# Kernel optimization log

Hardware: AMD Instinct MI355X
Metric: run time of the kernel (lower is better)

## Reference

```python
import jax, jax.numpy as jnp
import numpy as np

NUM_HEADS = 16
NHID = 64
D = NUM_HEADS * NHID  # 1024, also keys/query/values dim and out_dim
SL, BS = 2048, 32


def setup_inputs() -> dict:
    key = jax.random.key(0)
    ks = jax.random.split(key, 7)
    s = 1.0 / np.sqrt(D)
    return {
        "query": jax.random.normal(ks[0], (BS, D), jnp.float32),
        "keys": jax.random.normal(ks[1], (SL, BS, D), jnp.float32),
        "values": jax.random.normal(ks[2], (SL, BS, D), jnp.float32),
        "Wq": jax.random.normal(ks[3], (D, D), jnp.float32) * s,
        "Wk": jax.random.normal(ks[4], (D, D), jnp.float32) * s,
        "Wv": jax.random.normal(ks[5], (D, D), jnp.float32) * s,
        "Wo": jax.random.normal(ks[6], (D, D), jnp.float32) * s,
    }


def reference(query, keys, values, Wq, Wk, Wv, Wo):
    sl, bs, _ = keys.shape
    qp = query @ Wq.T                       # [bs, H*nhid]
    kp = keys @ Wk.T                        # [sl, bs, H*nhid]
    vp = values @ Wv.T                      # [sl, bs, H*nhid]
    # elementwise multiplicative score, reduced per head
    dot = (qp * kp).reshape(sl, bs, NUM_HEADS, NHID).sum(-1) / np.sqrt(NHID)
    # NOTE: original uses log_softmax (not softmax) over the sequence dim
    w = jax.nn.log_softmax(dot, axis=0)[..., None]        # [sl, bs, H, 1]
    attn = (w * vp.reshape(sl, bs, NUM_HEADS, NHID)).sum(0)  # [bs, H, nhid]
    return attn.reshape(bs, -1) @ Wo.T                     # [bs, D]
```

## Files before the change

kernel.cpp:

```cpp
#include <hip/hip_runtime.h>

#define SL  2048
#define BSZ 32
#define DIM 1024
#define NH  16
#define HD  64

typedef __attribute__((ext_vector_type(4))) float f32x4;
typedef __attribute__((ext_vector_type(8))) short s16x8;

static __device__ __forceinline__ short f2bf(float f) {
    union { float f; unsigned u; } v; v.f = f;
    unsigned r = (v.u + 0x7fffu + ((v.u >> 16) & 1u)) >> 16;
    return (short)r;
}

template<bool DUAL>
__global__ __launch_bounds__(256) void k_gemm(const float* __restrict__ A,
                                              const float* __restrict__ A2,
                                              const float* __restrict__ W,
                                              float* __restrict__ O,
                                              int rmul, int hsel) {
    int oc = blockIdx.x & 15;
    int b  = blockIdx.x >> 4;
    int wv = __builtin_amdgcn_readfirstlane(threadIdx.x >> 6);
    int lane = threadIdx.x & 63;
    int o = oc * 64 + lane;
    int row = b * rmul + (hsel ? oc : 0);
    const float* arow  = A + (size_t)row * DIM + wv * 256;
    const float* a2row = DUAL ? (A2 + (size_t)row * DIM + wv * 256) : nullptr;
    const float* wrow  = W + (size_t)o * DIM + wv * 256;
    f32x4 acc = {0.f, 0.f, 0.f, 0.f};
#pragma unroll 4
    for (int k = 0; k < 256; k += 4) {
        f32x4 a = *(const f32x4*)(arow + k);
        if (DUAL) a += *(const f32x4*)(a2row + k);
        f32x4 w = *(const f32x4*)(wrow + k);
        acc += a * w;
    }
    __shared__ float red[4][64];
    red[wv][lane] = acc[0] + acc[1] + acc[2] + acc[3];
    __syncthreads();
    int t = threadIdx.x;
    if (t < 64)
        O[(size_t)b * DIM + oc * 64 + t] = red[0][t] + red[1][t] + red[2][t] + red[3][t];
}

__global__ __launch_bounds__(256) void k_ut(const float* __restrict__ qp,
                                            const float* __restrict__ Wk,
                                            short* __restrict__ u) {
    int idx = blockIdx.x;
    int jc = idx & 15;
    int h  = (idx >> 4) & 15;
    int bg = idx >> 8;
    int wv = __builtin_amdgcn_readfirstlane(threadIdx.x >> 6);
    int lane = threadIdx.x & 63;
    int b = bg * 4 + wv;
    int j = jc * 64 + lane;
    const float* qrow = qp + (size_t)b * DIM + h * HD;
    const float* wcol = Wk + (size_t)(h * HD) * DIM + j;
    float acc = 0.f;
#pragma unroll 8
    for (int i = 0; i < HD; ++i) acc += qrow[i] * wcol[(size_t)i * DIM];
    u[((size_t)(b * NH + h)) * DIM + j] = f2bf(acc * 0.125f);
}

__global__ __launch_bounds__(256, 4) void k_dot(const float* __restrict__ keys,
                                                const short* __restrict__ u,
                                                float* __restrict__ dot) {
    int b  = blockIdx.x & 31;
    int s0 = (blockIdx.x >> 5) * 64;
    __shared__ short ulds[NH][DIM + 8];
    {
        const uint4* src = (const uint4*)(u + (size_t)b * NH * DIM);
        for (int idx = threadIdx.x; idx < NH * DIM / 8; idx += 256) {
            int row = idx >> 7;
            int col = (idx & 127) * 8;
            *(uint4*)&ulds[row][col] = src[idx];
        }
    }
    __syncthreads();
    int lane = threadIdx.x & 63;
    int wave = threadIdx.x >> 6;
    int lrow = lane & 15;
    int kgrp = lane >> 4;
    f32x4 acc = {0.f, 0.f, 0.f, 0.f};
    const float* ka = keys + ((size_t)(s0 + wave * 16 + lrow) * BSZ + b) * DIM;
#pragma unroll 4
    for (int k0 = 0; k0 < DIM; k0 += 32) {
        int kj = k0 + kgrp * 8;
        s16x8 bf = *(const s16x8*)&ulds[lrow][kj];
        f32x4 a0 = *(const f32x4*)(ka + kj);
        f32x4 a1 = *(const f32x4*)(ka + kj + 4);
        s16x8 af;
        af[0]=f2bf(a0[0]); af[1]=f2bf(a0[1]); af[2]=f2bf(a0[2]); af[3]=f2bf(a0[3]);
        af[4]=f2bf(a1[0]); af[5]=f2bf(a1[1]); af[6]=f2bf(a1[2]); af[7]=f2bf(a1[3]);
        acc = __builtin_amdgcn_mfma_f32_16x16x32_bf16(af, bf, acc, 0, 0, 0);
    }
    size_t obase = ((size_t)b * SL + (s0 + wave * 16 + kgrp * 4)) * NH + lrow;
#pragma unroll
    for (int r = 0; r < 4; ++r)
        dot[obase + (size_t)r * NH] = acc[r];
}

__global__ __launch_bounds__(1024) void k_red(const float* __restrict__ dot,
                                              float* __restrict__ T) {
    int b = blockIdx.x, t = threadIdx.x;
    const f32x4* base = (const f32x4*)(dot + (size_t)b * SL * NH);
    __shared__ f32x4 red[1024];
    __shared__ float Mh[16];
    f32x4 m = {-1e30f, -1e30f, -1e30f, -1e30f};
#pragma unroll
    for (int k = 0; k < 8; ++k) {
        f32x4 v = base[t + k * 1024];
        m[0]=fmaxf(m[0],v[0]); m[1]=fmaxf(m[1],v[1]);
        m[2]=fmaxf(m[2],v[2]); m[3]=fmaxf(m[3],v[3]);
    }
    red[t] = m;
    __syncthreads();
    for (int s = 512; s >= 4; s >>= 1) {
        if (t < s) {
            f32x4 a = red[t], c = red[t + s];
            a[0]=fmaxf(a[0],c[0]); a[1]=fmaxf(a[1],c[1]);
            a[2]=fmaxf(a[2],c[2]); a[3]=fmaxf(a[3],c[3]);
            red[t] = a;
        }
        __syncthreads();
    }
    if (t < 4) { f32x4 mm = red[t]; for (int i = 0; i < 4; ++i) Mh[t*4+i] = mm[i]; }
    __syncthreads();
    int hq = t & 3;
    f32x4 M4;
    M4[0]=Mh[hq*4]; M4[1]=Mh[hq*4+1]; M4[2]=Mh[hq*4+2]; M4[3]=Mh[hq*4+3];
    f32x4 ssum = {0.f,0.f,0.f,0.f};
#pragma unroll
    for (int k = 0; k < 8; ++k) {
        f32x4 v = base[t + k * 1024];
        ssum[0]+=__expf(v[0]-M4[0]); ssum[1]+=__expf(v[1]-M4[1]);
        ssum[2]+=__expf(v[2]-M4[2]); ssum[3]+=__expf(v[3]-M4[3]);
    }
    __syncthreads();
    red[t] = ssum;
    __syncthreads();
    for (int s = 512; s >= 4; s >>= 1) {
        if (t < s) { f32x4 a = red[t]; a += red[t + s]; red[t] = a; }
        __syncthreads();
    }
    if (t < 4) {
        f32x4 ss = red[t];
        for (int i = 0; i < 4; ++i)
            T[b * NH + t * 4 + i] = Mh[t * 4 + i] + __logf(ss[i]);
    }
}

__global__ __launch_bounds__(256, 4) void k_z(const float* __restrict__ values,
                                              const float* __restrict__ w,
                                              const float* __restrict__ T,
                                              float* __restrict__ z) {
    int x  = blockIdx.x;
    int b  = x & 31;
    int jc = (x >> 5) & 15;
    int sh = x >> 9;
    int t  = threadIdx.x;
    int ssub = t >> 4;
    int jq = t & 15;
    int j = jc * 64 + jq * 4;
    int wv = __builtin_amdgcn_readfirstlane(t >> 6);
    int lane = t & 63;

    __shared__ float wlds[128 * 16];
    __shared__ f32x4 redW[4][16][16];
    __shared__ f32x4 redV[4][16];

    f32x4 acc[NH];
#pragma unroll
    for (int h = 0; h < NH; ++h) acc[h] = (f32x4){0.f,0.f,0.f,0.f};
    f32x4 accV = {0.f,0.f,0.f,0.f};

    const float* vbase = values + (size_t)b * DIM + j;
    const float* wbase = w + ((size_t)b * SL + sh * 1024) * NH;

    for (int ph = 0; ph < 8; ++ph) {
        if (ph) __syncthreads();
        {
            const f32x4* src = (const f32x4*)(wbase + ph * 128 * NH);
            f32x4* dst = (f32x4*)wlds;
            dst[t]       = src[t];
            dst[t + 256] = src[t + 256];
        }
        __syncthreads();
        int sbase = sh * 1024 + ph * 128;
#pragma unroll 4
        for (int it = 0; it < 8; ++it) {
            int s_loc = it * 16 + ssub;
            f32x4 v = *(const f32x4*)(vbase + (size_t)(sbase + s_loc) * (BSZ * DIM));
            const float* wr = wlds + s_loc * 16;
#pragma unroll
            for (int h = 0; h < NH; ++h) {
                float wh = wr[h];
                acc[h] += v * wh;
            }
            accV += v;
        }
    }

#pragma unroll
    for (int h = 0; h < NH; ++h) {
#pragma unroll
        for (int e = 0; e < 4; ++e) {
            float x0 = acc[h][e];
            x0 += __shfl_xor(x0, 16);
            x0 += __shfl_xor(x0, 32);
            acc[h][e] = x0;
        }
    }
#pragma unroll
    for (int e = 0; e < 4; ++e) {
        float x0 = accV[e];
        x0 += __shfl_xor(x0, 16);
        x0 += __shfl_xor(x0, 32);
        accV[e] = x0;
    }
    if (lane < 16) {
#pragma unroll
        for (int h = 0; h < NH; ++h) redW[wv][h][lane] = acc[h];
        redV[wv][lane] = accV;
    }
    __syncthreads();
    int h2 = t >> 4, q = t & 15;
    f32x4 sumW = redW[0][h2][q] + redW[1][h2][q] + redW[2][h2][q] + redW[3][h2][q];
    f32x4 sumV = redV[0][q] + redV[1][q] + redV[2][q] + redV[3][q];
    float Th = T[b * NH + h2];
    f32x4 zv = sumW - Th * sumV;
    float* zp = z + (size_t)sh * (BSZ * NH * DIM);
    *(f32x4*)(zp + ((size_t)(b * NH + h2)) * DIM + jc * 64 + q * 4) = zv;
}

extern "C" void kernel_launch(void* const* d_in, const int* in_sizes, int n_in,
                              void* d_out, int out_size, void* d_ws, size_t ws_size,
                              hipStream_t stream) {
    const float* query  = (const float*)d_in[0];
    const float* keys   = (const float*)d_in[1];
    const float* values = (const float*)d_in[2];
    const float* Wq = (const float*)d_in[3];
    const float* Wk = (const float*)d_in[4];
    const float* Wv = (const float*)d_in[5];
    const float* Wo = (const float*)d_in[6];
    float* out = (float*)d_out;

    char* ws = (char*)d_ws;
    float* qp   = (float*)(ws + 0);
    short* u    = (short*)(ws + (128 << 10));
    float* dotb = (float*)(ws + (128 << 10) + (1 << 20));
    float* z0   = (float*)(ws + (128 << 10) + (5 << 20));
    float* z1   = (float*)(ws + (128 << 10) + (7 << 20));
    float* attn = (float*)(ws + (128 << 10) + (9 << 20));
    float* T    = (float*)(ws + (256 << 10) + (9 << 20));

    hipLaunchKernelGGL(k_gemm<false>, dim3(512),  dim3(256), 0, stream, query, nullptr, Wq, qp, 1, 0);
    hipLaunchKernelGGL(k_ut,          dim3(2048), dim3(256), 0, stream, qp, Wk, u);
    hipLaunchKernelGGL(k_dot,         dim3(1024), dim3(256), 0, stream, keys, u, dotb);
    hipLaunchKernelGGL(k_red,         dim3(32),   dim3(1024),0, stream, dotb, T);
    hipLaunchKernelGGL(k_z,           dim3(1024), dim3(256), 0, stream, values, dotb, T, z0);
    hipLaunchKernelGGL(k_gemm<true>,  dim3(512),  dim3(256), 0, stream, z0, z1, Wv, attn, 16, 1);
    hipLaunchKernelGGL(k_gemm<false>, dim3(512),  dim3(256), 0, stream, attn, nullptr, Wo, out, 1, 0);
}
```

Baseline: 199.1 us.

## Fuse query projection with u compute and fold softmax stats into dot kernel

Merges the Wq projection and the Wk-folded u computation into one kernel (k_qu). The dot kernel now also emits per-tile max and sum-exp partials, and k_z combines these online to get the log-sum-exp, which removes the separate k_red pass over the dot buffer. k_z also prefetches the next weight tile into registers and reads the per-row weights as vector LDS loads. The result is two fewer launches and one fewer full read of the dot scores, at the cost of some redundant partial combining in every k_z block.

```diff
diff --git a/kernel.cpp b/kernel.cpp
--- a/kernel.cpp
+++ b/kernel.cpp
@@ -13,6 +13,207 @@
     union { float f; unsigned u; } v; v.f = f;
     unsigned r = (v.u + 0x7fffu + ((v.u >> 16) & 1u)) >> 16;
     return (short)r;
+}
+
+__global__ __launch_bounds__(256) void k_qu(const float* __restrict__ query,
+                                            const float* __restrict__ Wq,
+                                            const float* __restrict__ Wk,
+                                            short* __restrict__ u) {
+    int b = blockIdx.x & 31;
+    int h = blockIdx.x >> 5;
+    int t = threadIdx.x;
+    __shared__ float red[256];
+    __shared__ float sq[HD];
+    {
+        int i  = t >> 2;
+        int kq = t & 3;
+        const float* q = query + (size_t)b * DIM + kq * 256;
+        const float* w = Wq + (size_t)(h * HD + i) * DIM + kq * 256;
+        f32x4 acc = {0.f, 0.f, 0.f, 0.f};
+#pragma unroll 4
+        for (int k = 0; k < 256; k += 4)
+            acc += *(const f32x4*)(q + k) * *(const f32x4*)(w + k);
+        red[t] = acc[0] + acc[1] + acc[2] + acc[3];
+    }
+    __syncthreads();
+    if (t < HD) sq[t] = (red[t*4] + red[t*4+1] + red[t*4+2] + red[t*4+3]) * 0.125f;
+    __syncthreads();
+    f32x4 acc = {0.f, 0.f, 0.f, 0.f};
+    const float* wk = Wk + (size_t)(h * HD) * DIM;
+#pragma unroll 8
+    for (int i = 0; i < HD; ++i) {
+        float s = sq[i];
+        const float* row = wk + (size_t)i * DIM;
+        acc[0] += s * row[t];
+        acc[1] += s * row[t + 256];
+        acc[2] += s * row[t + 512];
+        acc[3] += s * row[t + 768];
+    }
+    short* ub = u + ((size_t)(b * NH + h)) * DIM;
+    ub[t]       = f2bf(acc[0]);
+    ub[t + 256] = f2bf(acc[1]);
+    ub[t + 512] = f2bf(acc[2]);
+    ub[t + 768] = f2bf(acc[3]);
+}
+
+__global__ __launch_bounds__(256, 4) void k_dot(const float* __restrict__ keys,
+                                                const short* __restrict__ u,
+                                                float* __restrict__ dot,
+                                                float2* __restrict__ part) {
+    int b  = blockIdx.x & 31;
+    int st = blockIdx.x >> 5;
+    int s0 = st * 64;
+    __shared__ short ulds[NH][DIM + 8];
+    {
+        const uint4* src = (const uint4*)(u + (size_t)b * NH * DIM);
+        for (int idx = threadIdx.x; idx < NH * DIM / 8; idx += 256) {
+            int row = idx >> 7;
+            int col = (idx & 127) * 8;
+            *(uint4*)&ulds[row][col] = src[idx];
+        }
+    }
+    __syncthreads();
+    int lane = threadIdx.x & 63;
+    int wave = threadIdx.x >> 6;
+    int lrow = lane & 15;
+    int kgrp = lane >> 4;
+    f32x4 acc = {0.f, 0.f, 0.f, 0.f};
+    const float* ka = keys + ((size_t)(s0 + wave * 16 + lrow) * BSZ + b) * DIM;
+#pragma unroll 4
+    for (int k0 = 0; k0 < DIM; k0 += 32) {
+        int kj = k0 + kgrp * 8;
+        s16x8 bf = *(const s16x8*)&ulds[lrow][kj];
+        f32x4 a0 = *(const f32x4*)(ka + kj);
+        f32x4 a1 = *(const f32x4*)(ka + kj + 4);
+        s16x8 af;
+        af[0]=f2bf(a0[0]); af[1]=f2bf(a0[1]); af[2]=f2bf(a0[2]); af[3]=f2bf(a0[3]);
+        af[4]=f2bf(a1[0]); af[5]=f2bf(a1[1]); af[6]=f2bf(a1[2]); af[7]=f2bf(a1[3]);
+        acc = __builtin_amdgcn_mfma_f32_16x16x32_bf16(af, bf, acc, 0, 0, 0);
+    }
+    size_t obase = ((size_t)b * SL + (s0 + wave * 16 + kgrp * 4)) * NH + lrow;
+#pragma unroll
+    for (int r = 0; r < 4; ++r)
+        dot[obase + (size_t)r * NH] = acc[r];
+
+    __shared__ float mred[4][16], lred[4][16];
+    float m = fmaxf(fmaxf(acc[0], acc[1]), fmaxf(acc[2], acc[3]));
+    m = fmaxf(m, __shfl_xor(m, 16));
+    m = fmaxf(m, __shfl_xor(m, 32));
+    if (lane < 16) mred[wave][lrow] = m;
+    __syncthreads();
+    float mb = fmaxf(fmaxf(mred[0][lrow], mred[1][lrow]),
+                     fmaxf(mred[2][lrow], mred[3][lrow]));
+    float l = __expf(acc[0]-mb) + __expf(acc[1]-mb) + __expf(acc[2]-mb) + __expf(acc[3]-mb);
+    l += __shfl_xor(l, 16);
+    l += __shfl_xor(l, 32);
+    if (lane < 16) lred[wave][lrow] = l;
+    __syncthreads();
+    int t = threadIdx.x;
+    if (t < 16) {
+        float mbb = fmaxf(fmaxf(mred[0][t], mred[1][t]), fmaxf(mred[2][t], mred[3][t]));
+        float lb  = lred[0][t] + lred[1][t] + lred[2][t] + lred[3][t];
+        part[((size_t)b * 32 + st) * 16 + t] = make_float2(mbb, lb);
+    }
+}
+
+__global__ __launch_bounds__(256, 4) void k_z(const float* __restrict__ values,
+                                              const float* __restrict__ w,
+                                              const float2* __restrict__ part,
+                                              float* __restrict__ z) {
+    int x  = blockIdx.x;
+    int b  = x & 31;
+    int jc = (x >> 5) & 15;
+    int sh = x >> 9;
+    int t  = threadIdx.x;
+    int ssub = t >> 4;
+    int jq = t & 15;
+    int j = jc * 64 + jq * 4;
+    int wv = __builtin_amdgcn_readfirstlane(t >> 6);
+    int lane = t & 63;
+
+    __shared__ float wlds[128 * 16];
+    __shared__ float Tl[16];
+    __shared__ f32x4 redW[4][16][16];
+    __shared__ f32x4 redV[4][16];
+
+    if (t < 16) {
+        const float2* pb = part + (size_t)b * 32 * 16 + t;
+        float M = -1e30f;
+#pragma unroll
+        for (int i = 0; i < 32; ++i) M = fmaxf(M, pb[i * 16].x);
+        float L = 0.f;
+#pragma unroll
+        for (int i = 0; i < 32; ++i) { float2 p = pb[i * 16]; L += p.y * __expf(p.x - M); }
+        Tl[t] = M + __logf(L);
+    }
+
+    f32x4 acc[NH];
+#pragma unroll
+    for (int h = 0; h < NH; ++h) acc[h] = (f32x4){0.f,0.f,0.f,0.f};
+    f32x4 accV = {0.f,0.f,0.f,0.f};
+
+    const float* vbase = values + (size_t)b * DIM + j;
+    const float* wbase = w + ((size_t)b * SL + sh * 1024) * NH;
+
+    const f32x4* src = (const f32x4*)wbase;
+    f32x4 w0 = src[t], w1 = src[t + 256];
+
+    for (int ph = 0; ph < 8; ++ph) {
+        __syncthreads();
+        f32x4* dst = (f32x4*)wlds;
+        dst[t]       = w0;
+        dst[t + 256] = w1;
+        __syncthreads();
+        if (ph + 1 < 8) {
+            src += 512;
+            w0 = src[t];
+            w1 = src[t + 256];
+        }
+        int sbase = sh * 1024 + ph * 128;
+#pragma unroll 4
+        for (int it = 0; it < 8; ++it) {
+            int s_loc = it * 16 + ssub;
+            f32x4 v = *(const f32x4*)(vbase + (size_t)(sbase + s_loc) * (BSZ * DIM));
+            const f32x4* wr = (const f32x4*)(wlds + s_loc * 16);
+            f32x4 wv0 = wr[0], wv1 = wr[1], wv2 = wr[2], wv3 = wr[3];
+            acc[0]  += v * wv0[0]; acc[1]  += v * wv0[1]; acc[2]  += v * wv0[2]; acc[3]  += v * wv0[3];
+            acc[4]  += v * wv1[0]; acc[5]  += v * wv1[1]; acc[6]  += v * wv1[2]; acc[7]  += v * wv1[3];
+            acc[8]  += v * wv2[0]; acc[9]  += v * wv2[1]; acc[10] += v * wv2[2]; acc[11] += v * wv2[3];
+            acc[12] += v * wv3[0]; acc[13] += v * wv3[1]; acc[14] += v * wv3[2]; acc[15] += v * wv3[3];
+            accV += v;
+        }
+    }
+
+#pragma unroll
+    for (int h = 0; h < NH; ++h) {
+#pragma unroll
+        for (int e = 0; e < 4; ++e) {
+            float x0 = acc[h][e];
+            x0 += __shfl_xor(x0, 16);
+            x0 += __shfl_xor(x0, 32);
+            acc[h][e] = x0;
+        }
+    }
+#pragma unroll
+    for (int e = 0; e < 4; ++e) {
+        float x0 = accV[e];
+        x0 += __shfl_xor(x0, 16);
+        x0 += __shfl_xor(x0, 32);
+        accV[e] = x0;
+    }
+    if (lane < 16) {
+#pragma unroll
+        for (int h = 0; h < NH; ++h) redW[wv][h][lane] = acc[h];
+        redV[wv][lane] = accV;
+    }
+    __syncthreads();
+    int h2 = t >> 4, q = t & 15;
+    f32x4 sumW = redW[0][h2][q] + redW[1][h2][q] + redW[2][h2][q] + redW[3][h2][q];
+    f32x4 sumV = redV[0][q] + redV[1][q] + redV[2][q] + redV[3][q];
+    float Th = Tl[h2];
+    f32x4 zv = sumW - Th * sumV;
+    float* zp = z + (size_t)sh * (BSZ * NH * DIM);
+    *(f32x4*)(zp + ((size_t)(b * NH + h2)) * DIM + jc * 64 + q * 4) = zv;
 }
 
 template<bool DUAL>
@@ -46,196 +247,6 @@
         O[(size_t)b * DIM + oc * 64 + t] = red[0][t] + red[1][t] + red[2][t] + red[3][t];
 }
 
-__global__ __launch_bounds__(256) void k_ut(const float* __restrict__ qp,
-                                            const float* __restrict__ Wk,
-                                            short* __restrict__ u) {
-    int idx = blockIdx.x;
-    int jc = idx & 15;
-    int h  = (idx >> 4) & 15;
-    int bg = idx >> 8;
-    int wv = __builtin_amdgcn_readfirstlane(threadIdx.x >> 6);
-    int lane = threadIdx.x & 63;
-    int b = bg * 4 + wv;
-    int j = jc * 64 + lane;
-    const float* qrow = qp + (size_t)b * DIM + h * HD;
-    const float* wcol = Wk + (size_t)(h * HD) * DIM + j;
-    float acc = 0.f;
-#pragma unroll 8
-    for (int i = 0; i < HD; ++i) acc += qrow[i] * wcol[(size_t)i * DIM];
-    u[((size_t)(b * NH + h)) * DIM + j] = f2bf(acc * 0.125f);
-}
-
-__global__ __launch_bounds__(256, 4) void k_dot(const float* __restrict__ keys,
-                                                const short* __restrict__ u,
-                                                float* __restrict__ dot) {
-    int b  = blockIdx.x & 31;
-    int s0 = (blockIdx.x >> 5) * 64;
-    __shared__ short ulds[NH][DIM + 8];
-    {
-        const uint4* src = (const uint4*)(u + (size_t)b * NH * DIM);
-        for (int idx = threadIdx.x; idx < NH * DIM / 8; idx += 256) {
-            int row = idx >> 7;
-            int col = (idx & 127) * 8;
-            *(uint4*)&ulds[row][col] = src[idx];
-        }
-    }
-    __syncthreads();
-    int lane = threadIdx.x & 63;
-    int wave = threadIdx.x >> 6;
-    int lrow = lane & 15;
-    int kgrp = lane >> 4;
-    f32x4 acc = {0.f, 0.f, 0.f, 0.f};
-    const float* ka = keys + ((size_t)(s0 + wave * 16 + lrow) * BSZ + b) * DIM;
-#pragma unroll 4
-    for (int k0 = 0; k0 < DIM; k0 += 32) {
-        int kj = k0 + kgrp * 8;
-        s16x8 bf = *(const s16x8*)&ulds[lrow][kj];
-        f32x4 a0 = *(const f32x4*)(ka + kj);
-        f32x4 a1 = *(const f32x4*)(ka + kj + 4);
-        s16x8 af;
-        af[0]=f2bf(a0[0]); af[1]=f2bf(a0[1]); af[2]=f2bf(a0[2]); af[3]=f2bf(a0[3]);
-        af[4]=f2bf(a1[0]); af[5]=f2bf(a1[1]); af[6]=f2bf(a1[2]); af[7]=f2bf(a1[3]);
-        acc = __builtin_amdgcn_mfma_f32_16x16x32_bf16(af, bf, acc, 0, 0, 0);
-    }
-    size_t obase = ((size_t)b * SL + (s0 + wave * 16 + kgrp * 4)) * NH + lrow;
-#pragma unroll
-    for (int r = 0; r < 4; ++r)
-        dot[obase + (size_t)r * NH] = acc[r];
-}
-
-__global__ __launch_bounds__(1024) void k_red(const float* __restrict__ dot,
-                                              float* __restrict__ T) {
-    int b = blockIdx.x, t = threadIdx.x;
-    const f32x4* base = (const f32x4*)(dot + (size_t)b * SL * NH);
-    __shared__ f32x4 red[1024];
-    __shared__ float Mh[16];
-    f32x4 m = {-1e30f, -1e30f, -1e30f, -1e30f};
-#pragma unroll
-    for (int k = 0; k < 8; ++k) {
-        f32x4 v = base[t + k * 1024];
-        m[0]=fmaxf(m[0],v[0]); m[1]=fmaxf(m[1],v[1]);
-        m[2]=fmaxf(m[2],v[2]); m[3]=fmaxf(m[3],v[3]);
-    }
-    red[t] = m;
-    __syncthreads();
-    for (int s = 512; s >= 4; s >>= 1) {
-        if (t < s) {
-            f32x4 a = red[t], c = red[t + s];
-            a[0]=fmaxf(a[0],c[0]); a[1]=fmaxf(a[1],c[1]);
-            a[2]=fmaxf(a[2],c[2]); a[3]=fmaxf(a[3],c[3]);
-            red[t] = a;
-        }
-        __syncthreads();
-    }
-    if (t < 4) { f32x4 mm = red[t]; for (int i = 0; i < 4; ++i) Mh[t*4+i] = mm[i]; }
-    __syncthreads();
-    int hq = t & 3;
-    f32x4 M4;
-    M4[0]=Mh[hq*4]; M4[1]=Mh[hq*4+1]; M4[2]=Mh[hq*4+2]; M4[3]=Mh[hq*4+3];
-    f32x4 ssum = {0.f,0.f,0.f,0.f};
-#pragma unroll
-    for (int k = 0; k < 8; ++k) {
-        f32x4 v = base[t + k * 1024];
-        ssum[0]+=__expf(v[0]-M4[0]); ssum[1]+=__expf(v[1]-M4[1]);
-        ssum[2]+=__expf(v[2]-M4[2]); ssum[3]+=__expf(v[3]-M4[3]);
-    }
-    __syncthreads();
-    red[t] = ssum;
-    __syncthreads();
-    for (int s = 512; s >= 4; s >>= 1) {
-        if (t < s) { f32x4 a = red[t]; a += red[t + s]; red[t] = a; }
-        __syncthreads();
-    }
-    if (t < 4) {
-        f32x4 ss = red[t];
-        for (int i = 0; i < 4; ++i)
-            T[b * NH + t * 4 + i] = Mh[t * 4 + i] + __logf(ss[i]);
-    }
-}
-
-__global__ __launch_bounds__(256, 4) void k_z(const float* __restrict__ values,
-                                              const float* __restrict__ w,
-                                              const float* __restrict__ T,
-                                              float* __restrict__ z) {
-    int x  = blockIdx.x;
-    int b  = x & 31;
-    int jc = (x >> 5) & 15;
-    int sh = x >> 9;
-    int t  = threadIdx.x;
-    int ssub = t >> 4;
-    int jq = t & 15;
-    int j = jc * 64 + jq * 4;
-    int wv = __builtin_amdgcn_readfirstlane(t >> 6);
-    int lane = t & 63;
-
-    __shared__ float wlds[128 * 16];
-    __shared__ f32x4 redW[4][16][16];
-    __shared__ f32x4 redV[4][16];
-
-    f32x4 acc[NH];
-#pragma unroll
-    for (int h = 0; h < NH; ++h) acc[h] = (f32x4){0.f,0.f,0.f,0.f};
-    f32x4 accV = {0.f,0.f,0.f,0.f};
-
-    const float* vbase = values + (size_t)b * DIM + j;
-    const float* wbase = w + ((size_t)b * SL + sh * 1024) * NH;
-
-    for (int ph = 0; ph < 8; ++ph) {
-        if (ph) __syncthreads();
-        {
-            const f32x4* src = (const f32x4*)(wbase + ph * 128 * NH);
-            f32x4* dst = (f32x4*)wlds;
-            dst[t]       = src[t];
-            dst[t + 256] = src[t + 256];
-        }
-        __syncthreads();
-        int sbase = sh * 1024 + ph * 128;
-#pragma unroll 4
-        for (int it = 0; it < 8; ++it) {
-            int s_loc = it * 16 + ssub;
-            f32x4 v = *(const f32x4*)(vbase + (size_t)(sbase + s_loc) * (BSZ * DIM));
-            const float* wr = wlds + s_loc * 16;
-#pragma unroll
-            for (int h = 0; h < NH; ++h) {
-                float wh = wr[h];
-                acc[h] += v * wh;
-            }
-            accV += v;
-        }
-    }
-
-#pragma unroll
-    for (int h = 0; h < NH; ++h) {
-#pragma unroll
-        for (int e = 0; e < 4; ++e) {
-            float x0 = acc[h][e];
-            x0 += __shfl_xor(x0, 16);
-            x0 += __shfl_xor(x0, 32);
-            acc[h][e] = x0;
-        }
-    }
-#pragma unroll
-    for (int e = 0; e < 4; ++e) {
-        float x0 = accV[e];
-        x0 += __shfl_xor(x0, 16);
-        x0 += __shfl_xor(x0, 32);
-        accV[e] = x0;
-    }
-    if (lane < 16) {
-#pragma unroll
-        for (int h = 0; h < NH; ++h) redW[wv][h][lane] = acc[h];
-        redV[wv][lane] = accV;
-    }
-    __syncthreads();
-    int h2 = t >> 4, q = t & 15;
-    f32x4 sumW = redW[0][h2][q] + redW[1][h2][q] + redW[2][h2][q] + redW[3][h2][q];
-    f32x4 sumV = redV[0][q] + redV[1][q] + redV[2][q] + redV[3][q];
-    float Th = T[b * NH + h2];
-    f32x4 zv = sumW - Th * sumV;
-    float* zp = z + (size_t)sh * (BSZ * NH * DIM);
-    *(f32x4*)(zp + ((size_t)(b * NH + h2)) * DIM + jc * 64 + q * 4) = zv;
-}
-
 extern "C" void kernel_launch(void* const* d_in, const int* in_sizes, int n_in,
                               void* d_out, int out_size, void* d_ws, size_t ws_size,
                               hipStream_t stream) {
@@ -249,19 +260,16 @@
     float* out = (float*)d_out;
 
     char* ws = (char*)d_ws;
-    float* qp   = (float*)(ws + 0);
-    short* u    = (short*)(ws + (128 << 10));
-    float* dotb = (float*)(ws + (128 << 10) + (1 << 20));
-    float* z0   = (float*)(ws + (128 << 10) + (5 << 20));
-    float* z1   = (float*)(ws + (128 << 10) + (7 << 20));
-    float* attn = (float*)(ws + (128 << 10) + (9 << 20));
-    float* T    = (float*)(ws + (256 << 10) + (9 << 20));
-
-    hipLaunchKernelGGL(k_gemm<false>, dim3(512),  dim3(256), 0, stream, query, nullptr, Wq, qp, 1, 0);
-    hipLaunchKernelGGL(k_ut,          dim3(2048), dim3(256), 0, stream, qp, Wk, u);
-    hipLaunchKernelGGL(k_dot,         dim3(1024), dim3(256), 0, stream, keys, u, dotb);
-    hipLaunchKernelGGL(k_red,         dim3(32),   dim3(1024),0, stream, dotb, T);
-    hipLaunchKernelGGL(k_z,           dim3(1024), dim3(256), 0, stream, values, dotb, T, z0);
+    short*  u    = (short*)(ws + 0);
+    float*  dotb = (float*)(ws + (1 << 20));
+    float*  z0   = (float*)(ws + (5 << 20));
+    float*  z1   = (float*)(ws + (7 << 20));
+    float*  attn = (float*)(ws + (9 << 20));
+    float2* part = (float2*)(ws + (9 << 20) + (128 << 10));
+
+    hipLaunchKernelGGL(k_qu,          dim3(512),  dim3(256), 0, stream, query, Wq, Wk, u);
+    hipLaunchKernelGGL(k_dot,         dim3(1024), dim3(256), 0, stream, keys, u, dotb, part);
+    hipLaunchKernelGGL(k_z,           dim3(1024), dim3(256), 0, stream, values, dotb, part, z0);
     hipLaunchKernelGGL(k_gemm<true>,  dim3(512),  dim3(256), 0, stream, z0, z1, Wv, attn, 16, 1);
     hipLaunchKernelGGL(k_gemm<false>, dim3(512),  dim3(256), 0, stream, attn, nullptr, Wo, out, 1, 0);
 }
```

New measurement: 229.4 us. 15.2% more time.
